# Kernel optimization log

Measured on AMD Instinct MI355X. Metric: run time of the kernel, lower is better.

The kernel has to match this reference:

```python
import jax, jax.numpy as jnp
import numpy as np

N_NODES = 50000


def _gcn_conv(x, row, col, W, b, n_nodes):
    # symmetric-norm GCN conv with self loops already appended to (row, col)
    deg = jax.ops.segment_sum(jnp.ones_like(row, dtype=x.dtype), row, num_segments=n_nodes)
    # every node has a self loop, so deg >= 1; pow(-0.5) is finite
    dis = deg ** -0.5
    norm = dis[row] * dis[col]                       # [E']
    msg = x[row] * norm[:, None]                     # gather + scale  [E', d]
    agg = jax.ops.segment_sum(msg, col, num_segments=n_nodes)  # scatter-add [N, d]
    return agg @ W + b


def setup_inputs() -> dict:
    key = jax.random.key(0)
    ks = jax.random.split(key, 12)
    N, E, Q, d_in, h = N_NODES, 800000, 200000, 64, 128
    x = jax.random.normal(ks[0], (N, d_in), dtype=jnp.float32)
    edge_index = jax.random.randint(ks[1], (2, E), 0, N)
    edge_label_index = jax.random.randint(ks[2], (2, Q), 0, N)
    def lin(k, fan_in, fan_out):
        kw, kb = jax.random.split(k)
        bound = 1.0 / np.sqrt(fan_in)
        W = jax.random.uniform(kw, (fan_in, fan_out), minval=-bound, maxval=bound, dtype=jnp.float32)
        b = jax.random.uniform(kb, (fan_out,), minval=-bound, maxval=bound, dtype=jnp.float32)
        return W, b
    W1, b1 = lin(ks[3], d_in, h)
    W2, b2 = lin(ks[4], h, h)
    Wc1, bc1 = lin(ks[5], 2 * h, h)
    Wc2, bc2 = lin(ks[6], h, 1)
    return {"x": x, "edge_index": edge_index, "edge_label_index": edge_label_index,
            "W1": W1, "b1": b1, "W2": W2, "b2": b2,
            "Wc1": Wc1, "bc1": bc1, "Wc2": Wc2, "bc2": bc2}


def reference(x, edge_index, edge_label_index, W1, b1, W2, b2, Wc1, bc1, Wc2, bc2):
    n = x.shape[0]
    loops = jnp.arange(n, dtype=edge_index.dtype)
    row = jnp.concatenate([edge_index[0], loops])
    col = jnp.concatenate([edge_index[1], loops])
    h1 = jax.nn.relu(_gcn_conv(x, row, col, W1, b1, n))
    h2 = _gcn_conv(h1, row, col, W2, b2, n)
    src, dst = edge_label_index[0], edge_label_index[1]
    h = jnp.concatenate([h2[src], h2[dst]], axis=1)  # [Q, 2*hidden]
    h = jax.nn.relu(h @ Wc1 + bc1)
    return h @ Wc2 + bc2                              # [Q, 1]
```

## Files before the change

### kernel.cpp

```cpp
#include <hip/hip_runtime.h>


#define HB 128
#define NWIN 16384

typedef __attribute__((ext_vector_type(8))) short short8;
typedef __attribute__((ext_vector_type(4))) float floatx4;

static __device__ __forceinline__ unsigned int f2bf(float v) {
    union { float f; unsigned int u; } c; c.f = v;
    unsigned int lsb = (c.u >> 16) & 1u;
    c.u += 0x7FFFu + lsb;
    return c.u >> 16;
}
static __device__ __forceinline__ float bf2f(unsigned int h) {
    union { float f; unsigned int u; } c; c.u = h << 16;
    return c.f;
}
static __device__ __forceinline__ void store_split4(float4 v,
                                                    unsigned short* hi,
                                                    unsigned short* lo) {
    unsigned int h0 = f2bf(v.x), h1 = f2bf(v.y), h2 = f2bf(v.z), h3 = f2bf(v.w);
    uint2 hw; hw.x = h0 | (h1 << 16); hw.y = h2 | (h3 << 16);
    unsigned int l0 = f2bf(v.x - bf2f(h0)), l1 = f2bf(v.y - bf2f(h1));
    unsigned int l2 = f2bf(v.z - bf2f(h2)), l3 = f2bf(v.w - bf2f(h3));
    uint2 lw; lw.x = l0 | (l1 << 16); lw.y = l2 | (l3 << 16);
    *(uint2*)hi = hw;
    *(uint2*)lo = lw;
}

__global__ __launch_bounds__(256) void k_hist(const int* __restrict__ row,
                                              const int* __restrict__ col,
                                              unsigned int* __restrict__ hRow,
                                              unsigned int* __restrict__ hCol,
                                              int E, int W, int chunk) {
    __shared__ unsigned int lds[NWIN];
    int t = threadIdx.x, b = blockIdx.x;
    int p = blockIdx.y >> 1;
    int win = blockIdx.y & 1;
    int base = win * NWIN;
    int wcap = min(W - base, NWIN);
    if (wcap <= 0) return;
    const int* idxArr = p ? col : row;
    unsigned int* outArr = p ? hCol : hRow;
    int e0 = b * chunk, e1 = min(E, e0 + chunk);
    for (int i = t; i < wcap; i += 256) lds[i] = 0;
    __syncthreads();
    for (int e = e0 + t; e < e1; e += 256) {
        int idx = idxArr[e];
        int w = (idx >> 1) - base;
        if ((unsigned)w < (unsigned)wcap)
            atomicAdd(&lds[w], 1u << ((idx & 1) * 16));
    }
    __syncthreads();
    for (int i = t; i < wcap; i += 256)
        outArr[(size_t)b * W + base + i] = lds[i];
}

__global__ __launch_bounds__(256) void k_reduce(const unsigned int* __restrict__ hRow,
                                                unsigned int* __restrict__ hCol,
                                                int* __restrict__ cntCol,
                                                float* __restrict__ dis,
                                                int N, int W) {
    int w = blockIdx.x * 256 + threadIdx.x;
    if (w >= W) return;
    unsigned int r0 = 0, r1 = 0, c0 = 0, c1 = 0;
#pragma unroll 8
    for (int b = 0; b < HB; b++) {
        size_t idx = (size_t)b * W + w;
        unsigned int hr = hRow[idx];
        unsigned int hc = hCol[idx];
        hCol[idx] = c0 | (c1 << 16);
        r0 += hr & 0xFFFFu; r1 += hr >> 16;
        c0 += hc & 0xFFFFu; c1 += hc >> 16;
    }
    int n0 = 2 * w, n1 = 2 * w + 1;
    cntCol[n0] = (int)c0;
    dis[n0] = 1.0f / sqrtf((float)(r0 + 1));
    if (n1 < N) {
        cntCol[n1] = (int)c1;
        dis[n1] = 1.0f / sqrtf((float)(r1 + 1));
    }
}

__global__ __launch_bounds__(256) void k_scan1(const int* __restrict__ cnt,
                                               int* __restrict__ offs,
                                               int* __restrict__ bsum, int N) {
    __shared__ int ts[256];
    int t = threadIdx.x;
    int base = blockIdx.x * 1024 + t * 4;
    int v0 = (base + 0 < N) ? cnt[base + 0] : 0;
    int v1 = (base + 1 < N) ? cnt[base + 1] : 0;
    int v2 = (base + 2 < N) ? cnt[base + 2] : 0;
    int v3 = (base + 3 < N) ? cnt[base + 3] : 0;
    int sum = v0 + v1 + v2 + v3;
    ts[t] = sum;
    __syncthreads();
    for (int off = 1; off < 256; off <<= 1) {
        int x = (t >= off) ? ts[t - off] : 0;
        __syncthreads();
        ts[t] += x;
        __syncthreads();
    }
    int e = ts[t] - sum;
    if (base + 0 < N) offs[base + 0] = e;
    if (base + 1 < N) offs[base + 1] = e + v0;
    if (base + 2 < N) offs[base + 2] = e + v0 + v1;
    if (base + 3 < N) offs[base + 3] = e + v0 + v1 + v2;
    if (t == 255) bsum[blockIdx.x] = ts[255];
}

__global__ __launch_bounds__(256) void k_scan2(int* __restrict__ bsum, int B) {
    __shared__ int ts[256];
    int t = threadIdx.x;
    int v = (t < B) ? bsum[t] : 0;
    ts[t] = v;
    __syncthreads();
    for (int off = 1; off < 256; off <<= 1) {
        int x = (t >= off) ? ts[t - off] : 0;
        __syncthreads();
        ts[t] += x;
        __syncthreads();
    }
    if (t < B) bsum[t] = ts[t] - v;
}

__global__ __launch_bounds__(256) void k_scan3(int* __restrict__ offs,
                                               const int* __restrict__ bsum,
                                               int N, int E) {
    int i = blockIdx.x * 256 + threadIdx.x;
    if (i < N) offs[i] = offs[i] + bsum[i >> 10];
    if (i == 0) offs[N] = E;
}

__global__ __launch_bounds__(256) void k_fill3(const int* __restrict__ row,
                                               const int* __restrict__ col,
                                               const int* __restrict__ offs,
                                               const unsigned int* __restrict__ hCol,
                                               int* __restrict__ srcSorted,
                                               int E, int N, int W, int chunk) {
    __shared__ int base[NWIN];
    int t = threadIdx.x, b = blockIdx.x;
    int n0 = blockIdx.y * NWIN;
    int nCnt = min(NWIN, N - n0);
    int e0 = b * chunk, e1 = min(E, e0 + chunk);
    for (int wl = t; wl * 2 < nCnt; wl += 256) {
        unsigned int pref = hCol[(size_t)b * W + (n0 >> 1) + wl];
        int nn = n0 + wl * 2;
        base[wl * 2] = offs[nn] + (int)(pref & 0xFFFFu);
        if (wl * 2 + 1 < nCnt)
            base[wl * 2 + 1] = offs[nn + 1] + (int)(pref >> 16);
    }
    __syncthreads();
    for (int e = e0 + t; e < e1; e += 256) {
        int c = col[e] - n0;
        if ((unsigned)c < (unsigned)nCnt) {
            int pos = atomicAdd(&base[c], 1);
            srcSorted[pos] = row[e];
        }
    }
}

__global__ __launch_bounds__(256) void k_xb(const float* __restrict__ x,
                                            unsigned int* __restrict__ xb, int nWords) {
    int i = blockIdx.x * 256 + threadIdx.x;
    if (i < nWords) {
        float2 v = ((const float2*)x)[i];
        xb[i] = f2bf(v.x) | (f2bf(v.y) << 16);
    }
}

__global__ __launch_bounds__(256) void k_gather1(const unsigned short* __restrict__ s,
                                                 const int* __restrict__ offs,
                                                 const int* __restrict__ srcs,
                                                 const float* __restrict__ dis,
                                                 unsigned short* __restrict__ aggHi,
                                                 unsigned short* __restrict__ aggLo,
                                                 int N) {
    int tid = blockIdx.x * 256 + threadIdx.x;
    int node = tid >> 4;
    if (node >= N) return;
    int c4 = (tid & 15) * 4;
    int e = offs[node], eEnd = offs[node + 1];
    float dn = dis[node];
    uint2 w = *(const uint2*)(s + (size_t)node * 64 + c4);
    float4 acc;
    acc.x = bf2f(w.x & 0xFFFF) * dn; acc.y = bf2f(w.x >> 16) * dn;
    acc.z = bf2f(w.y & 0xFFFF) * dn; acc.w = bf2f(w.y >> 16) * dn;
    int srcNext = (e < eEnd) ? srcs[e] : 0;
    float dNext = dis[srcNext];
    while (e < eEnd) {
        int src = srcNext;
        float dsrc = dNext;
        e++;
        srcNext = (e < eEnd) ? srcs[e] : 0;
        dNext = dis[srcNext];
        uint2 v = *(const uint2*)(s + (size_t)src * 64 + c4);
        acc.x += bf2f(v.x & 0xFFFF) * dsrc; acc.y += bf2f(v.x >> 16) * dsrc;
        acc.z += bf2f(v.y & 0xFFFF) * dsrc; acc.w += bf2f(v.y >> 16) * dsrc;
    }
    acc.x *= dn; acc.y *= dn; acc.z *= dn; acc.w *= dn;
    store_split4(acc, aggHi + (size_t)node * 64 + c4, aggLo + (size_t)node * 64 + c4);
}

__global__ __launch_bounds__(256) void k_gather2(const unsigned short* __restrict__ s,
                                                 const int* __restrict__ offs,
                                                 const int* __restrict__ srcs,
                                                 const float* __restrict__ dis,
                                                 unsigned short* __restrict__ agg,
                                                 int N) {
    int tid = blockIdx.x * 256 + threadIdx.x;
    int node = tid >> 4;
    if (node >= N) return;
    int c8 = (tid & 15) * 8;
    int e = offs[node], eEnd = offs[node + 1];
    float dn = dis[node];
    uint4 w = *(const uint4*)(s + (size_t)node * 128 + c8);
    float a0 = bf2f(w.x & 0xFFFF), a1 = bf2f(w.x >> 16);
    float a2 = bf2f(w.y & 0xFFFF), a3 = bf2f(w.y >> 16);
    float a4 = bf2f(w.z & 0xFFFF), a5 = bf2f(w.z >> 16);
    float a6 = bf2f(w.w & 0xFFFF), a7 = bf2f(w.w >> 16);
    int srcNext = (e < eEnd) ? srcs[e] : 0;
    while (e < eEnd) {
        int src = srcNext;
        e++;
        srcNext = (e < eEnd) ? srcs[e] : 0;
        uint4 v = *(const uint4*)(s + (size_t)src * 128 + c8);
        a0 += bf2f(v.x & 0xFFFF); a1 += bf2f(v.x >> 16);
        a2 += bf2f(v.y & 0xFFFF); a3 += bf2f(v.y >> 16);
        a4 += bf2f(v.z & 0xFFFF); a5 += bf2f(v.z >> 16);
        a6 += bf2f(v.w & 0xFFFF); a7 += bf2f(v.w >> 16);
    }
    uint4 o;
    o.x = f2bf(a0 * dn) | (f2bf(a1 * dn) << 16);
    o.y = f2bf(a2 * dn) | (f2bf(a3 * dn) << 16);
    o.z = f2bf(a4 * dn) | (f2bf(a5 * dn) << 16);
    o.w = f2bf(a6 * dn) | (f2bf(a7 * dn) << 16);
    *(uint4*)(agg + (size_t)node * 128 + c8) = o;
}

__global__ __launch_bounds__(256) void k_fold(const float* __restrict__ W1,
                                              const float* __restrict__ W2,
                                              const float* __restrict__ Wc1,
                                              const float* __restrict__ b2,
                                              const float* __restrict__ bc1,
                                              unsigned short* __restrict__ UVhi,
                                              unsigned short* __restrict__ UVlo,
                                              unsigned short* __restrict__ W1hi,
                                              unsigned short* __restrict__ W1lo,
                                              float* __restrict__ buv) {
    __shared__ float w2row[128];
    int t = threadIdx.x, b = blockIdx.x;
    if (b < 128) {
        int k = b;
        int j = t & 127, half = t >> 7;
        int n = half * 128 + j;
        const float* wc = Wc1 + (size_t)half * 128 * 128 + j;
        if (t < 128) w2row[t] = W2[k * 128 + t];
        __syncthreads();
        float acc = 0.f;
#pragma unroll 8
        for (int m = 0; m < 128; m++) acc += w2row[m] * wc[(size_t)m * 128];
        int kstep = k >> 5, kl = k & 31, quad = kl >> 3, j8 = kl & 7;
        int nb = n >> 4, l = quad * 16 + (n & 15);
        int pidx = ((kstep * 16 + nb) * 64 + l) * 8 + j8;
        unsigned int h = f2bf(acc);
        UVhi[pidx] = (unsigned short)h;
        UVlo[pidx] = (unsigned short)f2bf(acc - bf2f(h));
    } else if (b == 128) {
        int j = t & 127, half = t >> 7;
        const float* wc = Wc1 + (size_t)half * 128 * 128 + j;
        float acc = half ? 0.f : bc1[j];
#pragma unroll 8
        for (int m = 0; m < 128; m++) acc += b2[m] * wc[(size_t)m * 128];
        buv[half * 128 + j] = acc;
    } else {
        int idx = (b - 129) * 256 + t;
        int k = idx >> 7, n = idx & 127;
        float v = W1[k * 128 + n];
        int kstep = k >> 5, kl = k & 31, quad = kl >> 3, j8 = kl & 7;
        int nb = n >> 4, l = quad * 16 + (n & 15);
        int pidx = ((kstep * 8 + nb) * 64 + l) * 8 + j8;
        unsigned int h = f2bf(v);
        W1hi[pidx] = (unsigned short)h;
        W1lo[pidx] = (unsigned short)f2bf(v - bf2f(h));
    }
}

__global__ __launch_bounds__(256) void k_mfma1(const unsigned short* __restrict__ Ahi,
                                               const unsigned short* __restrict__ Alo,
                                               const unsigned short* __restrict__ Bhi,
                                               const unsigned short* __restrict__ Blo,
                                               const float* __restrict__ b1,
                                               const float* __restrict__ dis,
                                               unsigned short* __restrict__ h1b, int N) {
    int lane = threadIdx.x & 63, wave = threadIdx.x >> 6;
    int quad = lane >> 4;
    short8 bh[2][2], bl[2][2];
#pragma unroll
    for (int ks = 0; ks < 2; ks++)
#pragma unroll
        for (int nt = 0; nt < 2; nt++) {
            int nb = wave * 2 + nt;
            bh[ks][nt] = *(const short8*)(Bhi + ((ks * 8 + nb) * 64 + lane) * 8);
            bl[ks][nt] = *(const short8*)(Blo + ((ks * 8 + nb) * 64 + lane) * 8);
        }
#pragma unroll
    for (int g = 0; g < 4; g++) {
        int mbase = blockIdx.x * 64 + g * 16;
        int ma = mbase + (lane & 15); if (ma >= N) ma = N - 1;
        floatx4 acc[2] = {};
#pragma unroll
        for (int ks = 0; ks < 2; ks++) {
            short8 ahi = *(const short8*)(Ahi + (size_t)ma * 64 + ks * 32 + quad * 8);
            short8 alo = *(const short8*)(Alo + (size_t)ma * 64 + ks * 32 + quad * 8);
#pragma unroll
            for (int nt = 0; nt < 2; nt++) {
                acc[nt] = __builtin_amdgcn_mfma_f32_16x16x32_bf16(ahi, bh[ks][nt], acc[nt], 0, 0, 0);
                acc[nt] = __builtin_amdgcn_mfma_f32_16x16x32_bf16(ahi, bl[ks][nt], acc[nt], 0, 0, 0);
                acc[nt] = __builtin_amdgcn_mfma_f32_16x16x32_bf16(alo, bh[ks][nt], acc[nt], 0, 0, 0);
            }
        }
        int md = mbase + quad * 4;
#pragma unroll
        for (int nt = 0; nt < 2; nt++) {
            int n0 = (wave * 2 + nt) * 16 + (lane & 15);
            float bias = b1[n0];
#pragma unroll
            for (int r = 0; r < 4; r++) {
                int node = md + r;
                if (node < N)
                    h1b[(size_t)node * 128 + n0] =
                        (unsigned short)f2bf(fmaxf(acc[nt][r] + bias, 0.f) * dis[node]);
            }
        }
    }
}

__global__ __launch_bounds__(256) void k_mfmaUV(const unsigned short* __restrict__ A,
                                                const unsigned short* __restrict__ Bhi,
                                                const unsigned short* __restrict__ Blo,
                                                const float* __restrict__ buv,
                                                unsigned short* __restrict__ Ub,
                                                unsigned short* __restrict__ Vb, int N) {
    int lane = threadIdx.x & 63, wave = threadIdx.x >> 6;
    int quad = lane >> 4;
    short8 bh[4][4], bl[4][4];
#pragma unroll
    for (int ks = 0; ks < 4; ks++)
#pragma unroll
        for (int nt = 0; nt < 4; nt++) {
            int nb = wave * 4 + nt;
            bh[ks][nt] = *(const short8*)(Bhi + ((ks * 16 + nb) * 64 + lane) * 8);
            bl[ks][nt] = *(const short8*)(Blo + ((ks * 16 + nb) * 64 + lane) * 8);
        }
#pragma unroll
    for (int g = 0; g < 4; g++) {
        int mbase = blockIdx.x * 64 + g * 16;
        int ma = mbase + (lane & 15); if (ma >= N) ma = N - 1;
        floatx4 acc[4] = {};
#pragma unroll
        for (int ks = 0; ks < 4; ks++) {
            short8 a = *(const short8*)(A + (size_t)ma * 128 + ks * 32 + quad * 8);
#pragma unroll
            for (int nt = 0; nt < 4; nt++) {
                acc[nt] = __builtin_amdgcn_mfma_f32_16x16x32_bf16(a, bh[ks][nt], acc[nt], 0, 0, 0);
                acc[nt] = __builtin_amdgcn_mfma_f32_16x16x32_bf16(a, bl[ks][nt], acc[nt], 0, 0, 0);
            }
        }
        int md = mbase + quad * 4;
#pragma unroll
        for (int nt = 0; nt < 4; nt++) {
            int n0 = wave * 64 + nt * 16 + (lane & 15);
            float bias = buv[n0];
            unsigned short* dst = (n0 < 128) ? Ub : Vb;
            int cc = n0 & 127;
#pragma unroll
            for (int r = 0; r < 4; r++) {
                int node = md + r;
                if (node < N)
                    dst[(size_t)node * 128 + cc] =
                        (unsigned short)f2bf(acc[nt][r] + bias);
            }
        }
    }
}

__global__ __launch_bounds__(256) void k_head(const unsigned short* __restrict__ Ub,
                                              const unsigned short* __restrict__ Vb,
                                              const int* __restrict__ srcA,
                                              const int* __restrict__ dstA,
                                              const float* __restrict__ Wc2,
                                              const float* __restrict__ bc2,
                                              float* __restrict__ out, int Q) {
    int t = threadIdx.x;
    int q = blockIdx.x * 16 + (t >> 4);
    if (q >= Q) return;
    int l = t & 15;
    int s = srcA[q], d = dstA[q];
    uint4 u = *(const uint4*)(Ub + (size_t)s * 128 + l * 8);
    uint4 v = *(const uint4*)(Vb + (size_t)d * 128 + l * 8);
    const float4* w = (const float4*)(Wc2 + l * 8);
    float4 w0 = w[0], w1 = w[1];
    float acc = 0.f, z;
    z = fmaxf(bf2f(u.x & 0xFFFF) + bf2f(v.x & 0xFFFF), 0.f); acc += z * w0.x;
    z = fmaxf(bf2f(u.x >> 16)    + bf2f(v.x >> 16),    0.f); acc += z * w0.y;
    z = fmaxf(bf2f(u.y & 0xFFFF) + bf2f(v.y & 0xFFFF), 0.f); acc += z * w0.z;
    z = fmaxf(bf2f(u.y >> 16)    + bf2f(v.y >> 16),    0.f); acc += z * w0.w;
    z = fmaxf(bf2f(u.z & 0xFFFF) + bf2f(v.z & 0xFFFF), 0.f); acc += z * w1.x;
    z = fmaxf(bf2f(u.z >> 16)    + bf2f(v.z >> 16),    0.f); acc += z * w1.y;
    z = fmaxf(bf2f(u.w & 0xFFFF) + bf2f(v.w & 0xFFFF), 0.f); acc += z * w1.z;
    z = fmaxf(bf2f(u.w >> 16)    + bf2f(v.w >> 16),    0.f); acc += z * w1.w;
    acc += __shfl_xor(acc, 1);
    acc += __shfl_xor(acc, 2);
    acc += __shfl_xor(acc, 4);
    acc += __shfl_xor(acc, 8);
    if (l == 0) out[q] = acc + bc2[0];
}

extern "C" void kernel_launch(void* const* d_in, const int* in_sizes, int n_in,
                              void* d_out, int out_size, void* d_ws, size_t ws_size,
                              hipStream_t stream) {
    const float* x   = (const float*)d_in[0];
    const int*   ei  = (const int*)d_in[1];
    const int*   eli = (const int*)d_in[2];
    const float* W1  = (const float*)d_in[3];
    const float* b1  = (const float*)d_in[4];
    const float* W2  = (const float*)d_in[5];
    const float* b2  = (const float*)d_in[6];
    const float* Wc1 = (const float*)d_in[7];
    const float* bc1 = (const float*)d_in[8];
    const float* Wc2 = (const float*)d_in[9];
    const float* bc2 = (const float*)d_in[10];
    float* out = (float*)d_out;
    char* wsb = (char*)d_ws;

    const int N = in_sizes[0] / 64;
    const int E = in_sizes[1] / 2;
    const int Q = in_sizes[2] / 2;
    const int W = (N + 1) / 2;
    const int chunk = (E + HB - 1) / HB;
    const int nPass = (N + NWIN - 1) / NWIN;
    const int nWinH = (W + NWIN - 1) / NWIN;

    float* dis       = (float*)wsb;
    int*   offs      = (int*)wsb + 65536;
    int*   bsum      = (int*)wsb + 197120;
    int*   cntCol    = (int*)wsb + 197376;
    float* buv       = (float*)wsb + 262912;
    unsigned short* UVhi = (unsigned short*)((int*)wsb + 263168);
    unsigned short* UVlo = (unsigned short*)((int*)wsb + 279552);
    unsigned short* W1hi = (unsigned short*)((int*)wsb + 295936);
    unsigned short* W1lo = (unsigned short*)((int*)wsb + 300032);
    int*   srcSorted = (int*)wsb + 304128;
    unsigned short* agg1hi = (unsigned short*)((int*)wsb + 1104128);
    unsigned short* agg1lo = (unsigned short*)((int*)wsb + 2704128);
    unsigned short* h1b    = (unsigned short*)((int*)wsb + 4304128);
    unsigned short* agg2b  = (unsigned short*)((int*)wsb + 7504128);
    unsigned short* Vb = agg1hi;
    unsigned short* Ub = h1b;
    unsigned int* hRow = (unsigned int*)wsb + 10704128;
    unsigned int* hCol = (unsigned int*)wsb + 13904128;
    unsigned int* xb   = (unsigned int*)wsb + 10704128;

    const int* row  = ei;
    const int* col  = ei + E;
    const int* srcA = eli;
    const int* dstA = eli + Q;

    const int scanB = (N + 1023) / 1024;

    k_hist<<<dim3(HB, 2 * nWinH), 256, 0, stream>>>(row, col, hRow, hCol, E, W, chunk);
    k_reduce<<<(W + 255) / 256, 256, 0, stream>>>(hRow, hCol, cntCol, dis, N, W);
    k_scan1<<<scanB, 256, 0, stream>>>(cntCol, offs, bsum, N);
    k_scan2<<<1, 256, 0, stream>>>(bsum, scanB);
    k_scan3<<<(N + 255) / 256, 256, 0, stream>>>(offs, bsum, N, E);
    k_xb<<<(N * 32 + 255) / 256, 256, 0, stream>>>(x, xb, N * 32);
    k_fill3<<<dim3(HB, nPass), 256, 0, stream>>>(row, col, offs, hCol, srcSorted, E, N, W, chunk);
    k_fold<<<161, 256, 0, stream>>>(W1, W2, Wc1, b2, bc1, UVhi, UVlo, W1hi, W1lo, buv);
    k_gather1<<<((size_t)N * 16 + 255) / 256, 256, 0, stream>>>(
        (const unsigned short*)xb, offs, srcSorted, dis, agg1hi, agg1lo, N);
    k_mfma1<<<(N + 63) / 64, 256, 0, stream>>>(agg1hi, agg1lo, W1hi, W1lo, b1, dis, h1b, N);
    k_gather2<<<((size_t)N * 16 + 255) / 256, 256, 0, stream>>>(
        h1b, offs, srcSorted, dis, agg2b, N);
    k_mfmaUV<<<(N + 63) / 64, 256, 0, stream>>>(agg2b, UVhi, UVlo, buv, Ub, Vb, N);
    k_head<<<(Q + 15) / 16, 256, 0, stream>>>(Ub, Vb, srcA, dstA, Wc2, bc2, out, Q);
}
```

Measured before the change: 280.8 us.

## Fuse layer-1 gather with MFMA and merge preprocessing kernels into one launch

Merges the histogram, x-to-bf16 conversion and weight-folding kernels into a single k_pre launch with block-range dispatch. Fuses the first-layer neighbour gather with the MFMA GEMM via an LDS tile, so the hi/lo aggregate no longer goes through global memory. Also unrolls the gather loops by two edges to raise memory-level parallelism. It saves launches and the round trip of the split-precision aggregate, but the fused conv1 runs 64 nodes per block with a serial pass loop, and k_pre carries a 64 KB LDS allocation even on its lightweight blocks, which may lower occupancy.

```diff
diff --git a/kernel.cpp b/kernel.cpp
--- a/kernel.cpp
+++ b/kernel.cpp
@@ -17,44 +17,92 @@
     union { float f; unsigned int u; } c; c.u = h << 16;
     return c.f;
 }
-static __device__ __forceinline__ void store_split4(float4 v,
-                                                    unsigned short* hi,
-                                                    unsigned short* lo) {
-    unsigned int h0 = f2bf(v.x), h1 = f2bf(v.y), h2 = f2bf(v.z), h3 = f2bf(v.w);
-    uint2 hw; hw.x = h0 | (h1 << 16); hw.y = h2 | (h3 << 16);
-    unsigned int l0 = f2bf(v.x - bf2f(h0)), l1 = f2bf(v.y - bf2f(h1));
-    unsigned int l2 = f2bf(v.z - bf2f(h2)), l3 = f2bf(v.w - bf2f(h3));
-    uint2 lw; lw.x = l0 | (l1 << 16); lw.y = l2 | (l3 << 16);
-    *(uint2*)hi = hw;
-    *(uint2*)lo = lw;
-}
-
-__global__ __launch_bounds__(256) void k_hist(const int* __restrict__ row,
-                                              const int* __restrict__ col,
-                                              unsigned int* __restrict__ hRow,
-                                              unsigned int* __restrict__ hCol,
-                                              int E, int W, int chunk) {
+
+__global__ __launch_bounds__(256) void k_pre(const int* __restrict__ row,
+                                             const int* __restrict__ col,
+                                             unsigned int* __restrict__ hRow,
+                                             unsigned int* __restrict__ hCol,
+                                             const float* __restrict__ x,
+                                             unsigned int* __restrict__ xb,
+                                             const float* __restrict__ W1,
+                                             const float* __restrict__ W2,
+                                             const float* __restrict__ Wc1,
+                                             const float* __restrict__ b2,
+                                             const float* __restrict__ bc1,
+                                             unsigned short* __restrict__ UVhi,
+                                             unsigned short* __restrict__ UVlo,
+                                             unsigned short* __restrict__ W1hi,
+                                             unsigned short* __restrict__ W1lo,
+                                             float* __restrict__ buv,
+                                             int E, int N, int W, int chunk,
+                                             int nHist, int nXb) {
     __shared__ unsigned int lds[NWIN];
     int t = threadIdx.x, b = blockIdx.x;
-    int p = blockIdx.y >> 1;
-    int win = blockIdx.y & 1;
-    int base = win * NWIN;
-    int wcap = min(W - base, NWIN);
-    if (wcap <= 0) return;
-    const int* idxArr = p ? col : row;
-    unsigned int* outArr = p ? hCol : hRow;
-    int e0 = b * chunk, e1 = min(E, e0 + chunk);
-    for (int i = t; i < wcap; i += 256) lds[i] = 0;
-    __syncthreads();
-    for (int e = e0 + t; e < e1; e += 256) {
-        int idx = idxArr[e];
-        int w = (idx >> 1) - base;
-        if ((unsigned)w < (unsigned)wcap)
-            atomicAdd(&lds[w], 1u << ((idx & 1) * 16));
-    }
-    __syncthreads();
-    for (int i = t; i < wcap; i += 256)
-        outArr[(size_t)b * W + base + i] = lds[i];
+    if (b < nHist) {
+        int hb = b % HB;
+        int yb = b / HB;
+        int p = yb >> 1, win = yb & 1;
+        int base = win * NWIN;
+        int wcap = min(W - base, NWIN);
+        if (wcap <= 0) return;
+        const int* idxArr = p ? col : row;
+        unsigned int* outArr = p ? hCol : hRow;
+        int e0 = hb * chunk, e1 = min(E, e0 + chunk);
+        for (int i = t; i < wcap; i += 256) lds[i] = 0;
+        __syncthreads();
+        for (int e = e0 + t; e < e1; e += 256) {
+            int idx = idxArr[e];
+            int w = (idx >> 1) - base;
+            if ((unsigned)w < (unsigned)wcap)
+                atomicAdd(&lds[w], 1u << ((idx & 1) * 16));
+        }
+        __syncthreads();
+        for (int i = t; i < wcap; i += 256)
+            outArr[(size_t)hb * W + base + i] = lds[i];
+    } else if (b < nHist + nXb) {
+        int i = (b - nHist) * 256 + t;
+        if (i < N * 32) {
+            float2 v = ((const float2*)x)[i];
+            xb[i] = f2bf(v.x) | (f2bf(v.y) << 16);
+        }
+    } else {
+        int bf = b - nHist - nXb;
+        float* w2row = (float*)lds;
+        if (bf < 128) {
+            int k = bf;
+            int j = t & 127, half = t >> 7;
+            int n = half * 128 + j;
+            const float* wc = Wc1 + (size_t)half * 128 * 128 + j;
+            if (t < 128) w2row[t] = W2[k * 128 + t];
+            __syncthreads();
+            float acc = 0.f;
+#pragma unroll 8
+            for (int m = 0; m < 128; m++) acc += w2row[m] * wc[(size_t)m * 128];
+            int kstep = k >> 5, kl = k & 31, quad = kl >> 3, j8 = kl & 7;
+            int nb = n >> 4, l = quad * 16 + (n & 15);
+            int pidx = ((kstep * 16 + nb) * 64 + l) * 8 + j8;
+            unsigned int h = f2bf(acc);
+            UVhi[pidx] = (unsigned short)h;
+            UVlo[pidx] = (unsigned short)f2bf(acc - bf2f(h));
+        } else if (bf == 128) {
+            int j = t & 127, half = t >> 7;
+            const float* wc = Wc1 + (size_t)half * 128 * 128 + j;
+            float acc = half ? 0.f : bc1[j];
+#pragma unroll 8
+            for (int m = 0; m < 128; m++) acc += b2[m] * wc[(size_t)m * 128];
+            buv[half * 128 + j] = acc;
+        } else {
+            int idx = (bf - 129) * 256 + t;
+            int k = idx >> 7, n = idx & 127;
+            float v = W1[k * 128 + n];
+            int kstep = k >> 5, kl = k & 31, quad = kl >> 3, j8 = kl & 7;
+            int nb = n >> 4, l = quad * 16 + (n & 15);
+            int pidx = ((kstep * 8 + nb) * 64 + l) * 8 + j8;
+            unsigned int h = f2bf(v);
+            W1hi[pidx] = (unsigned short)h;
+            W1lo[pidx] = (unsigned short)f2bf(v - bf2f(h));
+        }
+    }
 }
 
 __global__ __launch_bounds__(256) void k_reduce(const unsigned int* __restrict__ hRow,
@@ -161,46 +209,99 @@
     }
 }
 
-__global__ __launch_bounds__(256) void k_xb(const float* __restrict__ x,
-                                            unsigned int* __restrict__ xb, int nWords) {
-    int i = blockIdx.x * 256 + threadIdx.x;
-    if (i < nWords) {
-        float2 v = ((const float2*)x)[i];
-        xb[i] = f2bf(v.x) | (f2bf(v.y) << 16);
-    }
-}
-
-__global__ __launch_bounds__(256) void k_gather1(const unsigned short* __restrict__ s,
-                                                 const int* __restrict__ offs,
-                                                 const int* __restrict__ srcs,
-                                                 const float* __restrict__ dis,
-                                                 unsigned short* __restrict__ aggHi,
-                                                 unsigned short* __restrict__ aggLo,
-                                                 int N) {
-    int tid = blockIdx.x * 256 + threadIdx.x;
-    int node = tid >> 4;
-    if (node >= N) return;
-    int c4 = (tid & 15) * 4;
-    int e = offs[node], eEnd = offs[node + 1];
-    float dn = dis[node];
-    uint2 w = *(const uint2*)(s + (size_t)node * 64 + c4);
-    float4 acc;
-    acc.x = bf2f(w.x & 0xFFFF) * dn; acc.y = bf2f(w.x >> 16) * dn;
-    acc.z = bf2f(w.y & 0xFFFF) * dn; acc.w = bf2f(w.y >> 16) * dn;
-    int srcNext = (e < eEnd) ? srcs[e] : 0;
-    float dNext = dis[srcNext];
-    while (e < eEnd) {
-        int src = srcNext;
-        float dsrc = dNext;
-        e++;
-        srcNext = (e < eEnd) ? srcs[e] : 0;
-        dNext = dis[srcNext];
-        uint2 v = *(const uint2*)(s + (size_t)src * 64 + c4);
-        acc.x += bf2f(v.x & 0xFFFF) * dsrc; acc.y += bf2f(v.x >> 16) * dsrc;
-        acc.z += bf2f(v.y & 0xFFFF) * dsrc; acc.w += bf2f(v.y >> 16) * dsrc;
-    }
-    acc.x *= dn; acc.y *= dn; acc.z *= dn; acc.w *= dn;
-    store_split4(acc, aggHi + (size_t)node * 64 + c4, aggLo + (size_t)node * 64 + c4);
+__global__ __launch_bounds__(256) void k_conv1(const unsigned short* __restrict__ s,
+                                               const int* __restrict__ offs,
+                                               const int* __restrict__ srcs,
+                                               const float* __restrict__ dis,
+                                               const unsigned short* __restrict__ Bhi,
+                                               const unsigned short* __restrict__ Blo,
+                                               const float* __restrict__ b1,
+                                               unsigned short* __restrict__ h1b, int N) {
+    __shared__ unsigned short Ahi[64][72];
+    __shared__ unsigned short Alo[64][72];
+    int t = threadIdx.x;
+    int lane = t & 63, wave = t >> 6;
+    int quad = lane >> 4;
+    short8 bh[2][2], bl[2][2];
+#pragma unroll
+    for (int ks = 0; ks < 2; ks++)
+#pragma unroll
+        for (int nt = 0; nt < 2; nt++) {
+            int nb = wave * 2 + nt;
+            bh[ks][nt] = *(const short8*)(Bhi + ((ks * 8 + nb) * 64 + lane) * 8);
+            bl[ks][nt] = *(const short8*)(Blo + ((ks * 8 + nb) * 64 + lane) * 8);
+        }
+#pragma unroll
+    for (int pass = 0; pass < 4; pass++) {
+        int nl = pass * 16 + (t >> 4);
+        int node = blockIdx.x * 64 + nl;
+        if (node < N) {
+            int c4 = (t & 15) * 4;
+            int e = offs[node], eEnd = offs[node + 1];
+            float dn = dis[node];
+            uint2 w = *(const uint2*)(s + (size_t)node * 64 + c4);
+            float4 acc;
+            acc.x = bf2f(w.x & 0xFFFF) * dn; acc.y = bf2f(w.x >> 16) * dn;
+            acc.z = bf2f(w.y & 0xFFFF) * dn; acc.w = bf2f(w.y >> 16) * dn;
+            while (e + 1 < eEnd) {
+                int sA = srcs[e], sB = srcs[e + 1];
+                float dA = dis[sA], dB = dis[sB];
+                uint2 vA = *(const uint2*)(s + (size_t)sA * 64 + c4);
+                uint2 vB = *(const uint2*)(s + (size_t)sB * 64 + c4);
+                acc.x += bf2f(vA.x & 0xFFFF) * dA + bf2f(vB.x & 0xFFFF) * dB;
+                acc.y += bf2f(vA.x >> 16) * dA + bf2f(vB.x >> 16) * dB;
+                acc.z += bf2f(vA.y & 0xFFFF) * dA + bf2f(vB.y & 0xFFFF) * dB;
+                acc.w += bf2f(vA.y >> 16) * dA + bf2f(vB.y >> 16) * dB;
+                e += 2;
+            }
+            if (e < eEnd) {
+                int sA = srcs[e];
+                float dA = dis[sA];
+                uint2 vA = *(const uint2*)(s + (size_t)sA * 64 + c4);
+                acc.x += bf2f(vA.x & 0xFFFF) * dA; acc.y += bf2f(vA.x >> 16) * dA;
+                acc.z += bf2f(vA.y & 0xFFFF) * dA; acc.w += bf2f(vA.y >> 16) * dA;
+            }
+            acc.x *= dn; acc.y *= dn; acc.z *= dn; acc.w *= dn;
+            unsigned int h0 = f2bf(acc.x), h1 = f2bf(acc.y),
+                         h2 = f2bf(acc.z), h3 = f2bf(acc.w);
+            uint2 hw; hw.x = h0 | (h1 << 16); hw.y = h2 | (h3 << 16);
+            uint2 lw;
+            lw.x = f2bf(acc.x - bf2f(h0)) | (f2bf(acc.y - bf2f(h1)) << 16);
+            lw.y = f2bf(acc.z - bf2f(h2)) | (f2bf(acc.w - bf2f(h3)) << 16);
+            *(uint2*)(&Ahi[nl][c4]) = hw;
+            *(uint2*)(&Alo[nl][c4]) = lw;
+        }
+    }
+    __syncthreads();
+#pragma unroll
+    for (int g = 0; g < 4; g++) {
+        int ml = g * 16 + (lane & 15);
+        floatx4 acc[2] = {};
+#pragma unroll
+        for (int ks = 0; ks < 2; ks++) {
+            short8 ahi = *(const short8*)(&Ahi[ml][ks * 32 + quad * 8]);
+            short8 alo = *(const short8*)(&Alo[ml][ks * 32 + quad * 8]);
+#pragma unroll
+            for (int nt = 0; nt < 2; nt++) {
+                acc[nt] = __builtin_amdgcn_mfma_f32_16x16x32_bf16(ahi, bh[ks][nt], acc[nt], 0, 0, 0);
+                acc[nt] = __builtin_amdgcn_mfma_f32_16x16x32_bf16(ahi, bl[ks][nt], acc[nt], 0, 0, 0);
+                acc[nt] = __builtin_amdgcn_mfma_f32_16x16x32_bf16(alo, bh[ks][nt], acc[nt], 0, 0, 0);
+            }
+        }
+        int md = blockIdx.x * 64 + g * 16 + quad * 4;
+#pragma unroll
+        for (int nt = 0; nt < 2; nt++) {
+            int n0 = (wave * 2 + nt) * 16 + (lane & 15);
+            float bias = b1[n0];
+#pragma unroll
+            for (int r = 0; r < 4; r++) {
+                int node = md + r;
+                if (node < N)
+                    h1b[(size_t)node * 128 + n0] =
+                        (unsigned short)f2bf(fmaxf(acc[nt][r] + bias, 0.f) * dis[node]);
+            }
+        }
+    }
 }
 
 __global__ __launch_bounds__(256) void k_gather2(const unsigned short* __restrict__ s,
@@ -220,16 +321,27 @@
     float a2 = bf2f(w.y & 0xFFFF), a3 = bf2f(w.y >> 16);
     float a4 = bf2f(w.z & 0xFFFF), a5 = bf2f(w.z >> 16);
     float a6 = bf2f(w.w & 0xFFFF), a7 = bf2f(w.w >> 16);
-    int srcNext = (e < eEnd) ? srcs[e] : 0;
-    while (e < eEnd) {
-        int src = srcNext;
-        e++;
-        srcNext = (e < eEnd) ? srcs[e] : 0;
-        uint4 v = *(const uint4*)(s + (size_t)src * 128 + c8);
-        a0 += bf2f(v.x & 0xFFFF); a1 += bf2f(v.x >> 16);
-        a2 += bf2f(v.y & 0xFFFF); a3 += bf2f(v.y >> 16);
-        a4 += bf2f(v.z & 0xFFFF); a5 += bf2f(v.z >> 16);
-        a6 += bf2f(v.w & 0xFFFF); a7 += bf2f(v.w >> 16);
+    while (e + 1 < eEnd) {
+        int sA = srcs[e], sB = srcs[e + 1];
+        uint4 vA = *(const uint4*)(s + (size_t)sA * 128 + c8);
+        uint4 vB = *(const uint4*)(s + (size_t)sB * 128 + c8);
+        a0 += bf2f(vA.x & 0xFFFF) + bf2f(vB.x & 0xFFFF);
+        a1 += bf2f(vA.x >> 16) + bf2f(vB.x >> 16);
+        a2 += bf2f(vA.y & 0xFFFF) + bf2f(vB.y & 0xFFFF);
+        a3 += bf2f(vA.y >> 16) + bf2f(vB.y >> 16);
+        a4 += bf2f(vA.z & 0xFFFF) + bf2f(vB.z & 0xFFFF);
+        a5 += bf2f(vA.z >> 16) + bf2f(vB.z >> 16);
+        a6 += bf2f(vA.w & 0xFFFF) + bf2f(vB.w & 0xFFFF);
+        a7 += bf2f(vA.w >> 16) + bf2f(vB.w >> 16);
+        e += 2;
+    }
+    if (e < eEnd) {
+        int sA = srcs[e];
+        uint4 vA = *(const uint4*)(s + (size_t)sA * 128 + c8);
+        a0 += bf2f(vA.x & 0xFFFF); a1 += bf2f(vA.x >> 16);
+        a2 += bf2f(vA.y & 0xFFFF); a3 += bf2f(vA.y >> 16);
+        a4 += bf2f(vA.z & 0xFFFF); a5 += bf2f(vA.z >> 16);
+        a6 += bf2f(vA.w & 0xFFFF); a7 += bf2f(vA.w >> 16);
     }
     uint4 o;
     o.x = f2bf(a0 * dn) | (f2bf(a1 * dn) << 16);
@@ -237,104 +349,6 @@
     o.z = f2bf(a4 * dn) | (f2bf(a5 * dn) << 16);
     o.w = f2bf(a6 * dn) | (f2bf(a7 * dn) << 16);
     *(uint4*)(agg + (size_t)node * 128 + c8) = o;
-}
-
-__global__ __launch_bounds__(256) void k_fold(const float* __restrict__ W1,
-                                              const float* __restrict__ W2,
-                                              const float* __restrict__ Wc1,
-                                              const float* __restrict__ b2,
-                                              const float* __restrict__ bc1,
-                                              unsigned short* __restrict__ UVhi,
-                                              unsigned short* __restrict__ UVlo,
-                                              unsigned short* __restrict__ W1hi,
-                                              unsigned short* __restrict__ W1lo,
-                                              float* __restrict__ buv) {
-    __shared__ float w2row[128];
-    int t = threadIdx.x, b = blockIdx.x;
-    if (b < 128) {
-        int k = b;
-        int j = t & 127, half = t >> 7;
-        int n = half * 128 + j;
-        const float* wc = Wc1 + (size_t)half * 128 * 128 + j;
-        if (t < 128) w2row[t] = W2[k * 128 + t];
-        __syncthreads();
-        float acc = 0.f;
-#pragma unroll 8
-        for (int m = 0; m < 128; m++) acc += w2row[m] * wc[(size_t)m * 128];
-        int kstep = k >> 5, kl = k & 31, quad = kl >> 3, j8 = kl & 7;
-        int nb = n >> 4, l = quad * 16 + (n & 15);
-        int pidx = ((kstep * 16 + nb) * 64 + l) * 8 + j8;
-        unsigned int h = f2bf(acc);
-        UVhi[pidx] = (unsigned short)h;
-        UVlo[pidx] = (unsigned short)f2bf(acc - bf2f(h));
-    } else if (b == 128) {
-        int j = t & 127, half = t >> 7;
-        const float* wc = Wc1 + (size_t)half * 128 * 128 + j;
-        float acc = half ? 0.f : bc1[j];
-#pragma unroll 8
-        for (int m = 0; m < 128; m++) acc += b2[m] * wc[(size_t)m * 128];
-        buv[half * 128 + j] = acc;
-    } else {
-        int idx = (b - 129) * 256 + t;
-        int k = idx >> 7, n = idx & 127;
-        float v = W1[k * 128 + n];
-        int kstep = k >> 5, kl = k & 31, quad = kl >> 3, j8 = kl & 7;
-        int nb = n >> 4, l = quad * 16 + (n & 15);
-        int pidx = ((kstep * 8 + nb) * 64 + l) * 8 + j8;
-        unsigned int h = f2bf(v);
-        W1hi[pidx] = (unsigned short)h;
-        W1lo[pidx] = (unsigned short)f2bf(v - bf2f(h));
-    }
-}
-
-__global__ __launch_bounds__(256) void k_mfma1(const unsigned short* __restrict__ Ahi,
-                                               const unsigned short* __restrict__ Alo,
-                                               const unsigned short* __restrict__ Bhi,
-                                               const unsigned short* __restrict__ Blo,
-                                               const float* __restrict__ b1,
-                                               const float* __restrict__ dis,
-                                               unsigned short* __restrict__ h1b, int N) {
-    int lane = threadIdx.x & 63, wave = threadIdx.x >> 6;
-    int quad = lane >> 4;
-    short8 bh[2][2], bl[2][2];
-#pragma unroll
-    for (int ks = 0; ks < 2; ks++)
-#pragma unroll
-        for (int nt = 0; nt < 2; nt++) {
-            int nb = wave * 2 + nt;
-            bh[ks][nt] = *(const short8*)(Bhi + ((ks * 8 + nb) * 64 + lane) * 8);
-            bl[ks][nt] = *(const short8*)(Blo + ((ks * 8 + nb) * 64 + lane) * 8);
-        }
-#pragma unroll
-    for (int g = 0; g < 4; g++) {
-        int mbase = blockIdx.x * 64 + g * 16;
-        int ma = mbase + (lane & 15); if (ma >= N) ma = N - 1;
-        floatx4 acc[2] = {};
-#pragma unroll
-        for (int ks = 0; ks < 2; ks++) {
-            short8 ahi = *(const short8*)(Ahi + (size_t)ma * 64 + ks * 32 + quad * 8);
-            short8 alo = *(const short8*)(Alo + (size_t)ma * 64 + ks * 32 + quad * 8);
-#pragma unroll
-            for (int nt = 0; nt < 2; nt++) {
-                acc[nt] = __builtin_amdgcn_mfma_f32_16x16x32_bf16(ahi, bh[ks][nt], acc[nt], 0, 0, 0);
-                acc[nt] = __builtin_amdgcn_mfma_f32_16x16x32_bf16(ahi, bl[ks][nt], acc[nt], 0, 0, 0);
-                acc[nt] = __builtin_amdgcn_mfma_f32_16x16x32_bf16(alo, bh[ks][nt], acc[nt], 0, 0, 0);
-            }
-        }
-        int md = mbase + quad * 4;
-#pragma unroll
-        for (int nt = 0; nt < 2; nt++) {
-            int n0 = (wave * 2 + nt) * 16 + (lane & 15);
-            float bias = b1[n0];
-#pragma unroll
-            for (int r = 0; r < 4; r++) {
-                int node = md + r;
-                if (node < N)
-                    h1b[(size_t)node * 128 + n0] =
-                        (unsigned short)f2bf(fmaxf(acc[nt][r] + bias, 0.f) * dis[node]);
-            }
-        }
-    }
 }
 
 __global__ __launch_bounds__(256) void k_mfmaUV(const unsigned short* __restrict__ A,
@@ -442,6 +456,8 @@
     const int chunk = (E + HB - 1) / HB;
     const int nPass = (N + NWIN - 1) / NWIN;
     const int nWinH = (W + NWIN - 1) / NWIN;
+    const int nHist = HB * 2 * nWinH;
+    const int nXb   = (N * 32 + 255) / 256;
 
     float* dis       = (float*)wsb;
     int*   offs      = (int*)wsb + 65536;
@@ -453,15 +469,13 @@
     unsigned short* W1hi = (unsigned short*)((int*)wsb + 295936);
     unsigned short* W1lo = (unsigned short*)((int*)wsb + 300032);
     int*   srcSorted = (int*)wsb + 304128;
-    unsigned short* agg1hi = (unsigned short*)((int*)wsb + 1104128);
-    unsigned short* agg1lo = (unsigned short*)((int*)wsb + 2704128);
-    unsigned short* h1b    = (unsigned short*)((int*)wsb + 4304128);
-    unsigned short* agg2b  = (unsigned short*)((int*)wsb + 7504128);
-    unsigned short* Vb = agg1hi;
+    unsigned short* Vb   = (unsigned short*)((int*)wsb + 1104128);
+    unsigned short* h1b  = (unsigned short*)((int*)wsb + 4304128);
+    unsigned short* agg2b= (unsigned short*)((int*)wsb + 7504128);
     unsigned short* Ub = h1b;
     unsigned int* hRow = (unsigned int*)wsb + 10704128;
     unsigned int* hCol = (unsigned int*)wsb + 13904128;
-    unsigned int* xb   = (unsigned int*)wsb + 10704128;
+    unsigned int* xb   = (unsigned int*)wsb + 17104128;
 
     const int* row  = ei;
     const int* col  = ei + E;
@@ -470,17 +484,16 @@
 
     const int scanB = (N + 1023) / 1024;
 
-    k_hist<<<dim3(HB, 2 * nWinH), 256, 0, stream>>>(row, col, hRow, hCol, E, W, chunk);
+    k_pre<<<nHist + nXb + 161, 256, 0, stream>>>(
+        row, col, hRow, hCol, x, xb, W1, W2, Wc1, b2, bc1,
+        UVhi, UVlo, W1hi, W1lo, buv, E, N, W, chunk, nHist, nXb);
     k_reduce<<<(W + 255) / 256, 256, 0, stream>>>(hRow, hCol, cntCol, dis, N, W);
     k_scan1<<<scanB, 256, 0, stream>>>(cntCol, offs, bsum, N);
     k_scan2<<<1, 256, 0, stream>>>(bsum, scanB);
     k_scan3<<<(N + 255) / 256, 256, 0, stream>>>(offs, bsum, N, E);
-    k_xb<<<(N * 32 + 255) / 256, 256, 0, stream>>>(x, xb, N * 32);
     k_fill3<<<dim3(HB, nPass), 256, 0, stream>>>(row, col, offs, hCol, srcSorted, E, N, W, chunk);
-    k_fold<<<161, 256, 0, stream>>>(W1, W2, Wc1, b2, bc1, UVhi, UVlo, W1hi, W1lo, buv);
-    k_gather1<<<((size_t)N * 16 + 255) / 256, 256, 0, stream>>>(
-        (const unsigned short*)xb, offs, srcSorted, dis, agg1hi, agg1lo, N);
-    k_mfma1<<<(N + 63) / 64, 256, 0, stream>>>(agg1hi, agg1lo, W1hi, W1lo, b1, dis, h1b, N);
+    k_conv1<<<(N + 63) / 64, 256, 0, stream>>>(
+        (const unsigned short*)xb, offs, srcSorted, dis, W1hi, W1lo, b1, h1b, N);
     k_gather2<<<((size_t)N * 16 + 255) / 256, 256, 0, stream>>>(
         h1b, offs, srcSorted, dis, agg2b, N);
     k_mfmaUV<<<(N + 63) / 64, 256, 0, stream>>>(agg2b, UVhi, UVlo, buv, Ub, Vb, N);
```

After: 280.5 us. About the same (-0.1%).
